# Performance work log

Measured on AMD Instinct MI355X. Metric: run time of the kernel, lower is better.

Reference implementation:

```python
import jax, jax.numpy as jnp
import numpy as np
import math

B, L, D = 8, 2048, 768
ORDER, EMB = 128, 5
FFT = 2 * L
MIN_DECAY = math.log(0.01) / 1.5   # slow_decay_pct = 1.5
MAX_DECAY = math.log(0.01) / 0.3   # fast_decay_pct = 0.3
SHIFT = 0.0


def _pos_emb(seq_len, emb_dim):
    # pos_emb_init from the source: [t, Re(z), Im(z)] with bands = (emb_dim-1)//2
    bands = (emb_dim - 1) // 2
    t = jnp.linspace(0.0, 1.0, seq_len)[None, :, None]
    t_res = jnp.linspace(0.0, seq_len - 1, seq_len)[None, :, None]
    w = 2.0 * jnp.pi * t_res / seq_len
    f = jnp.linspace(1e-4, bands - 1, bands)[None, None]
    zc = jnp.exp(-1j * f * w)
    return jnp.concatenate([t, zc.real, zc.imag], axis=-1).astype(jnp.float32)  # (1, L, EMB)


def setup_inputs() -> dict:
    key = jax.random.key(0)
    ks = jax.random.split(key, 16)
    s = 0.02
    return {
        "u": jax.random.normal(ks[0], (B, L, D), jnp.float32),
        "in_W": jax.random.normal(ks[1], (D, 3 * D), jnp.float32) * s,
        "in_b": jnp.zeros((3 * D,), jnp.float32),
        "out_W": jax.random.normal(ks[2], (D, D), jnp.float32) * s,
        "out_b": jnp.zeros((D,), jnp.float32),
        "x1_s": jax.random.normal(ks[3], (D, 4), jnp.float32) * 0.25,
        "x2_s": jax.random.normal(ks[4], (D, 4), jnp.float32) * 0.25,
        "v_s": jax.random.normal(ks[5], (D, 4), jnp.float32) * 0.25,
        "x1_sb": jax.random.normal(ks[6], (D,), jnp.float32) * 0.1,
        "x2_sb": jax.random.normal(ks[7], (D,), jnp.float32) * 0.1,
        "v_sb": jax.random.normal(ks[8], (D,), jnp.float32) * 0.1,
        "D_bias": jax.random.normal(ks[9], (D,), jnp.float32),
        "z": _pos_emb(L, EMB),
        "sin_freq": 10.0 * jnp.ones((1, ORDER), jnp.float32),   # hyena_w = 10
        "eo_mat": jax.random.normal(ks[10], (1, EMB, ORDER), jnp.float32) * 0.3,
        "eo_bias": jnp.zeros((1, ORDER), jnp.float32),
        "oo1_mat": jax.random.normal(ks[11], (1, ORDER, ORDER), jnp.float32) * 0.08,
        "oo1_bias": jnp.zeros((1, ORDER), jnp.float32),
        "oo2_mat": jax.random.normal(ks[12], (1, ORDER, ORDER), jnp.float32) * 0.08,
        "oo2_bias": jnp.zeros((1, ORDER), jnp.float32),
        "oh_mat": jax.random.normal(ks[13], (1, ORDER, D), jnp.float32) * 0.08,
    }


def _depthwise4(x, w, b):
    # torch Conv1d(groups=3D, kernel=4, padding=3) truncated to [:L] == causal conv, left pad 3
    out = jax.lax.conv_general_dilated(
        x, w[:, None, :], window_strides=(1,), padding=[(3, 0)],
        dimension_numbers=("NCH", "OIH", "NCH"), feature_group_count=x.shape[1])
    return out + b[None, :, None]


def _hyena_filter(z, sin_freq, eo_mat, eo_bias, oo1_mat, oo1_bias, oo2_mat, oo2_bias, oh_mat):
    # then exponential decay modulation (exp_mod_in_place_fwd), channels=1, reverse=0.
    f = sin_freq[:, None, :]                                       # (1, 1, ORDER)
    h = jnp.sin(f * (jnp.einsum("cle,ceo->clo", z, eo_mat) + eo_bias[:, None, :]))
    h = jnp.sin(f * (jnp.einsum("clo,cop->clp", h, oo1_mat) + oo1_bias[:, None, :]))
    h = jnp.sin(f * (jnp.einsum("clo,cop->clp", h, oo2_mat) + oo2_bias[:, None, :]))
    k = jnp.einsum("clo,coh->clh", h, oh_mat)                      # (1, L, D)
    t = jnp.linspace(0.0, 1.0, k.shape[1])
    deltas = jnp.abs(jnp.linspace(MIN_DECAY, MAX_DECAY, k.shape[2]))
    k = k * (jnp.exp(-t[None, :, None] * deltas[None, None, :]) + SHIFT)
    return k[0].T                                                  # (D, L)


def _forward(u, in_W, in_b, out_W, out_b, x1_s, x2_s, v_s, x1_sb, x2_sb, v_sb,
             D_bias, z, sin_freq, eo_mat, eo_bias, oo1_mat, oo1_bias,
             oo2_mat, oo2_bias, oh_mat):
    seqlen = u.shape[1]
    k = _hyena_filter(z, sin_freq, eo_mat, eo_bias, oo1_mat, oo1_bias, oo2_mat, oo2_bias, oh_mat)
    x1x2v = u @ in_W + in_b                                        # (B, L, 3D)
    x1, x2, v = jnp.split(x1x2v, 3, axis=-1)
    x1 = jnp.transpose(x1, (0, 2, 1))                              # (B, D, L)
    x2 = jnp.transpose(x2, (0, 2, 1))
    v = jnp.transpose(v, (0, 2, 1))
    x1 = _depthwise4(x1, x1_s, x1_sb)
    x2 = _depthwise4(x2, x2_s, x2_sb)
    v = _depthwise4(v, v_s, v_sb)
    v = v * x1                                                     # first gate
    k_f = jnp.fft.rfft(k.astype(jnp.float32), n=FFT)               # (D, FFT//2+1)
    v_f = jnp.fft.rfft(v.astype(jnp.float32), n=FFT)               # (B, D, FFT//2+1)
    y = jnp.fft.irfft(v_f * k_f[None], n=FFT)[..., :seqlen]        # long FFT conv
    y = y + v * D_bias[None, :, None]                              # skip term
    y = y * x2                                                     # second gate
    y = jnp.transpose(y, (0, 2, 1))                                # (B, L, D)
    return y @ out_W + out_b


def reference(u, in_W, in_b, out_W, out_b, x1_s, x2_s, v_s, x1_sb, x2_sb, v_sb,
              D_bias, z, sin_freq, eo_mat, eo_bias, oo1_mat, oo1_bias,
              oo2_mat, oo2_bias, oh_mat):
    return _forward(u, in_W, in_b, out_W, out_b, x1_s, x2_s, v_s, x1_sb, x2_sb, v_sb,
                    D_bias, z, sin_freq, eo_mat, eo_bias, oo1_mat, oo1_bias,
                    oo2_mat, oo2_bias, oh_mat)
```

## Files before the change

### kernel.cpp

```cpp
#include <hip/hip_runtime.h>


typedef __bf16 bf16x8 __attribute__((ext_vector_type(8)));
typedef float  f32x4  __attribute__((ext_vector_type(4)));

#define AS1 __attribute__((address_space(1)))
#define AS3 __attribute__((address_space(3)))
#define GLD16(gp, lp) __builtin_amdgcn_global_load_lds((AS1 void*)(void*)(gp), (AS3 void*)(void*)(lp), 16, 0, 0)

#define LGKM_BAR       __asm__ __volatile__("s_waitcnt lgkmcnt(0)\n\ts_barrier" ::: "memory")
#define VM_LGKM_BAR(N) __asm__ __volatile__("s_waitcnt vmcnt(" #N ") lgkmcnt(0)\n\ts_barrier" ::: "memory")

__device__ __forceinline__ unsigned short f2b(float f) {
    unsigned u = __builtin_bit_cast(unsigned, f);
    unsigned r = (u + 0x7fffu + ((u >> 16) & 1u)) >> 16;
    return (unsigned short)r;
}
__device__ __forceinline__ float b2f_lo(unsigned u) {
    return __builtin_bit_cast(float, u << 16);
}
__device__ __forceinline__ float b2f_hi(unsigned u) {
    return __builtin_bit_cast(float, u & 0xffff0000u);
}

__device__ __forceinline__ float2 cmul(float2 a, float2 b) {
    return make_float2(a.x * b.x - a.y * b.y, a.x * b.y + a.y * b.x);
}
__device__ __forceinline__ float2 cadd(float2 a, float2 b) { return make_float2(a.x + b.x, a.y + b.y); }
__device__ __forceinline__ float2 csub(float2 a, float2 b) { return make_float2(a.x - b.x, a.y - b.y); }

#define TWO_PI 6.283185307179586f

#define BFLY(i,j)   { float2 ta=x[i], tb=x[j]; x[i]=cadd(ta,tb); x[j]=csub(ta,tb); }
#define BFLYW(i,j,w){ float2 ta=x[i], tb=x[j]; x[i]=cadd(ta,tb); x[j]=cmul(csub(ta,tb),(w)); }
#define BFLYI(i,j)  { float2 ta=x[i], tb=x[j]; x[i]=cadd(ta,tb); float2 tt=csub(ta,tb); x[j]=make_float2(-dd*tt.y, dd*tt.x); }
#define CSWAP(i,j)  { float2 tt=x[i]; x[i]=x[j]; x[j]=tt; }

template<int DIR, bool UZ>
__device__ __forceinline__ void dft16(float2* x) {
    const float dd = (float)DIR;
    const float C1 = 0.92387953251128674f, S1 = 0.38268343236508977f, R2 = 0.70710678118654752f;
    const float2 W1 = make_float2( C1, dd*S1);
    const float2 W2 = make_float2( R2, dd*R2);
    const float2 W3 = make_float2( S1, dd*C1);
    const float2 W5 = make_float2(-S1, dd*C1);
    const float2 W6 = make_float2(-R2, dd*R2);
    const float2 W7 = make_float2(-C1, dd*S1);
    if (UZ) {
        x[8]  = x[0];
        x[9]  = cmul(x[1], W1);
        x[10] = cmul(x[2], W2);
        x[11] = cmul(x[3], W3);
        x[12] = make_float2(-dd*x[4].y, dd*x[4].x);
        x[13] = cmul(x[5], W5);
        x[14] = cmul(x[6], W6);
        x[15] = cmul(x[7], W7);
    } else {
        BFLY(0,8); BFLYW(1,9,W1); BFLYW(2,10,W2); BFLYW(3,11,W3);
        BFLYI(4,12); BFLYW(5,13,W5); BFLYW(6,14,W6); BFLYW(7,15,W7);
    }
    BFLY(0,4);  BFLYW(1,5,W2);  BFLYI(2,6);   BFLYW(3,7,W6);
    BFLY(8,12); BFLYW(9,13,W2); BFLYI(10,14); BFLYW(11,15,W6);
    BFLY(0,2);  BFLYI(1,3);  BFLY(4,6);   BFLYI(5,7);
    BFLY(8,10); BFLYI(9,11); BFLY(12,14); BFLYI(13,15);
    BFLY(0,1); BFLY(2,3); BFLY(4,5); BFLY(6,7);
    BFLY(8,9); BFLY(10,11); BFLY(12,13); BFLY(14,15);
    CSWAP(1,8); CSWAP(2,4); CSWAP(3,12); CSWAP(5,10); CSWAP(7,14); CSWAP(11,13);
}

__device__ __forceinline__ void twiddle16(float2* x, float ang) {
    float s, c; __sincosf(ang, &s, &c);
    const float2 u1  = make_float2(c, s);
    const float2 u2  = cmul(u1, u1);
    const float2 u3  = cmul(u2, u1);
    const float2 u4  = cmul(u2, u2);
    const float2 u8  = cmul(u4, u4);
    const float2 u12 = cmul(u8, u4);
    x[1]  = cmul(x[1],  u1);
    x[2]  = cmul(x[2],  u2);
    x[3]  = cmul(x[3],  u3);
    x[4]  = cmul(x[4],  u4);
    x[5]  = cmul(x[5],  cmul(u4, u1));
    x[6]  = cmul(x[6],  cmul(u4, u2));
    x[7]  = cmul(x[7],  cmul(u4, u3));
    x[8]  = cmul(x[8],  u8);
    x[9]  = cmul(x[9],  cmul(u8, u1));
    x[10] = cmul(x[10], cmul(u8, u2));
    x[11] = cmul(x[11], cmul(u8, u3));
    x[12] = cmul(x[12], u12);
    x[13] = cmul(x[13], cmul(u12, u1));
    x[14] = cmul(x[14], cmul(u12, u2));
    x[15] = cmul(x[15], cmul(u12, u3));
}

__device__ __forceinline__ int ph1(int row, int col) { return row * 256 + (col ^ row); }
__device__ __forceinline__ int ph2(int row, int col) { return row * 16 + (col ^ (row & 15)); }

__device__ __forceinline__ void fft4096_fwd(float2* x, float2* lds, int t) {
    dft16<-1, true>(x);
    twiddle16(x, -(float)t * (TWO_PI / 4096.0f));
    #pragma unroll
    for (int k1 = 0; k1 < 16; ++k1) lds[ph1(k1, t)] = x[k1];
    __syncthreads();
    const int hi = t >> 4, lo = t & 15;
    #pragma unroll
    for (int t1 = 0; t1 < 16; ++t1) x[t1] = lds[ph1(hi, t1 * 16 + lo)];
    dft16<-1, false>(x);
    twiddle16(x, -(float)lo * (TWO_PI / 256.0f));
    __syncthreads();
    #pragma unroll
    for (int k2 = 0; k2 < 16; ++k2) lds[ph2(t, k2)] = x[k2];
    __syncthreads();
    #pragma unroll
    for (int t0 = 0; t0 < 16; ++t0) x[t0] = lds[ph2(hi * 16 + t0, lo)];
    dft16<-1, false>(x);
}

__device__ __forceinline__ void fft4096_inv(float2* x, float2* lds, int t) {
    const int hi = t >> 4, lo = t & 15;
    dft16<1, false>(x);
    __syncthreads();
    #pragma unroll
    for (int t0 = 0; t0 < 16; ++t0) lds[ph2(hi * 16 + t0, lo)] = x[t0];
    __syncthreads();
    #pragma unroll
    for (int k2 = 0; k2 < 16; ++k2) x[k2] = lds[ph2(t, k2)];
    twiddle16(x, (float)lo * (TWO_PI / 256.0f));
    dft16<1, false>(x);
    __syncthreads();
    #pragma unroll
    for (int t1 = 0; t1 < 16; ++t1) lds[ph1(hi, t1 * 16 + lo)] = x[t1];
    __syncthreads();
    #pragma unroll
    for (int k1 = 0; k1 < 16; ++k1) x[k1] = lds[ph1(k1, t)];
    twiddle16(x, (float)t * (TWO_PI / 4096.0f));
    dft16<1, false>(x);
}

__global__ __launch_bounds__(256) void filter_k_kernel(
    const float* __restrict__ z, const float* __restrict__ sf,
    const float* __restrict__ eo, const float* __restrict__ eo_b,
    const float* __restrict__ oo1, const float* __restrict__ oo1_b,
    const float* __restrict__ oo2, const float* __restrict__ oo2_b,
    const float* __restrict__ oh, float* __restrict__ kfil)
{
    __shared__ float h3buf[4][128];
    __shared__ float htmp[2][128];
    const int t = threadIdx.x;
    const int l0 = blockIdx.x * 4;
    const int half = t >> 7;
    const int o = t & 127;
    const float sfo = sf[o];
    for (int p = 0; p < 2; ++p) {
        const int li = p * 2 + half;
        const int l = l0 + li;
        float a = eo_b[o];
        #pragma unroll
        for (int e = 0; e < 5; ++e) a += z[l * 5 + e] * eo[e * 128 + o];
        htmp[half][o] = sinf(sfo * a);
        __syncthreads();
        float a2 = oo1_b[o];
        for (int q = 0; q < 128; ++q) a2 += htmp[half][q] * oo1[q * 128 + o];
        const float h2 = sinf(sfo * a2);
        __syncthreads();
        htmp[half][o] = h2;
        __syncthreads();
        float a3 = oo2_b[o];
        for (int q = 0; q < 128; ++q) a3 += htmp[half][q] * oo2[q * 128 + o];
        h3buf[li][o] = sinf(sfo * a3);
        __syncthreads();
    }
    const float MIND = -3.070113457325394f;
    const float MAXD = -15.350567286626972f;
    for (int c = 0; c < 3; ++c) {
        const int h = t + c * 256;
        float acc[4];
        #pragma unroll
        for (int li = 0; li < 4; ++li) acc[li] = 0.f;
        for (int q = 0; q < 128; ++q) {
            const float w = oh[q * 768 + h];
            #pragma unroll
            for (int li = 0; li < 4; ++li) acc[li] += h3buf[li][q] * w;
        }
        const float delta = fabsf(MIND + (MAXD - MIND) * (float)h * (1.0f / 767.0f));
        #pragma unroll
        for (int li = 0; li < 4; ++li) {
            const int l = l0 + li;
            const float tt = (float)l * (1.0f / 2047.0f);
            kfil[h * 2048 + l] = acc[li] * expf(-tt * delta);
        }
    }
}

__global__ __launch_bounds__(256) void filter_fft_kernel(
    const float* __restrict__ kfil, const float* __restrict__ D_bias,
    float2* __restrict__ Kf)
{
    __shared__ __align__(16) float2 lds[4096];
    const int d = blockIdx.x, t = threadIdx.x;
    float2 x[16];
    #pragma unroll
    for (int r = 0; r < 8; ++r) x[r] = make_float2(kfil[d * 2048 + r * 256 + t], 0.f);
    fft4096_fwd(x, lds, t);
    const float db = D_bias[d];
    const float s = 1.0f / 4096.0f;
    #pragma unroll
    for (int k3 = 0; k3 < 16; ++k3)
        Kf[d * 4096 + k3 * 256 + t] = make_float2((x[k3].x + db) * s, x[k3].y * s);
}

__global__ __launch_bounds__(256) void convert_u_kernel(
    const float* __restrict__ u, unsigned short* __restrict__ ub)
{
    const int g = blockIdx.x * 256 + threadIdx.x;
    const float4 v = ((const float4*)u)[g];
    uint2 o;
    o.x = (unsigned)f2b(v.x) | ((unsigned)f2b(v.y) << 16);
    o.y = (unsigned)f2b(v.z) | ((unsigned)f2b(v.w) << 16);
    ((uint2*)ub)[g] = o;
}

__global__ __launch_bounds__(256) void transpose_W_kernel(
    const float* __restrict__ W, unsigned short* __restrict__ Wt, int K, int N)
{
    __shared__ float tile[32][33];
    const int n0 = blockIdx.x * 32, k0 = blockIdx.y * 32;
    const int tx = threadIdx.x & 31, ty = threadIdx.x >> 5;
    #pragma unroll
    for (int r = 0; r < 4; ++r) {
        const int kk = ty + r * 8;
        tile[kk][tx] = W[(k0 + kk) * N + n0 + tx];
    }
    __syncthreads();
    #pragma unroll
    for (int r = 0; r < 4; ++r) {
        const int nn = ty + r * 8;
        Wt[(n0 + nn) * K + k0 + tx] = f2b(tile[tx][nn]);
    }
}

__global__ __launch_bounds__(256) void transpose_Y_kernel(
    const unsigned short* __restrict__ Y, unsigned short* __restrict__ Yt)
{
    __shared__ unsigned short tile[32][34];
    const int bx = blockIdx.x;
    const int l0 = (bx & 63) * 32;
    const int tmp = bx >> 6;
    const int d0 = (tmp % 24) * 32;
    const int b  = tmp / 24;
    const int tx = threadIdx.x & 31, ty = threadIdx.x >> 5;
    #pragma unroll
    for (int r = 0; r < 4; ++r) {
        const int dd = ty + r * 8;
        tile[dd][tx] = Y[(b * 768 + d0 + dd) * 2048 + l0 + tx];
    }
    __syncthreads();
    #pragma unroll
    for (int r = 0; r < 4; ++r) {
        const int ll = ty + r * 8;
        Yt[(b * 2048 + l0 + ll) * 768 + d0 + tx] = tile[tx][ll];
    }
}

template<int TM, int TN, int WR, int WC, int MODE>
__global__ __launch_bounds__(512, 2) void gemm8ph_kernel(
    const unsigned short* __restrict__ A,
    const unsigned short* __restrict__ Bm,
    const float* __restrict__ bias,
    unsigned short* __restrict__ outb,
    float* __restrict__ outf)
{
    constexpr int MF = TM / WR / 16;
    constexpr int NF = TN / WC / 16;
    constexpr int MH = MF / 2;
    constexpr int NH = NF / 2;
    constexpr int QA = TM / 64;
    constexpr int QB = TN / 64;
    extern __shared__ __align__(16) unsigned short lds[];
    unsigned short* As = lds;
    unsigned short* Bs = lds + 2 * TM * 64;
    const int t = threadIdx.x;
    const int wv = t >> 6, lane = t & 63;
    const int row0 = (MODE == 0 ? blockIdx.y : blockIdx.x) * TM;
    const int col0 = (MODE == 0 ? blockIdx.x : blockIdx.y) * TN;
    const int wr = wv / WC, wc = wv % WC;
    const int frow = lane & 15, kc = lane >> 4;

    f32x4 acc[MF][NF] = {};

    const int srow = t >> 3;
    const int cdat = (t & 7) ^ (srow & 7);
    const unsigned short* gA = A  + (row0 + srow) * 768 + cdat * 8;
    const unsigned short* gB = Bm + (col0 + srow) * 768 + cdat * 8;

#define STG_Aq(buf, q, kt) GLD16(gA + (q) * 49152 + (kt),                     \
        (char*)As + (buf) * (TM * 128) + (q) * 8192 + wv * 1024)
#define STG_Bq(buf, q, kt) GLD16(gB + (q) * 49152 + (kt),                     \
        (char*)Bs + (buf) * (TN * 128) + (q) * 8192 + wv * 1024)
#define STG_A1(buf, kt) { STG_Aq(buf, 0, kt); STG_Aq(buf, 1, kt); }
#define STG_A2(buf, kt) { _Pragma("unroll") for (int q = 2; q < QA; ++q) STG_Aq(buf, q, kt); }
#define STG_B1(buf, kt) { STG_Bq(buf, 0, kt); STG_Bq(buf, 1, kt); }
#define STG_B2(buf, kt) { _Pragma("unroll") for (int q = 2; q < QB; ++q) STG_Bq(buf, q, kt); }
#define FENCE_QB { if constexpr (QB == 4) { VM_LGKM_BAR(4); } else { VM_LGKM_BAR(3); } }

    bf16x8 aF[MH][2], bN0[NH][2], bN1[NH][2];

#define READ_A(buf, mh)                                                        \
    _Pragma("unroll") for (int m = 0; m < MH; ++m) {                           \
        const int r = wr * (TM / WR) + ((mh) * MH + m) * 16 + frow;            \
        aF[m][0] = *(const bf16x8*)(As + (buf) * (TM * 64) + r * 64 +          \
                                    (((0 + kc) ^ (r & 7)) << 3));              \
        aF[m][1] = *(const bf16x8*)(As + (buf) * (TM * 64) + r * 64 +          \
                                    (((4 + kc) ^ (r & 7)) << 3));              \
    }
#define READ_B(buf, nh, arr)                                                   \
    _Pragma("unroll") for (int n = 0; n < NH; ++n) {                           \
        const int r = wc * (TN / WC) + ((nh) * NH + n) * 16 + frow;            \
        arr[n][0] = *(const bf16x8*)(Bs + (buf) * (TN * 64) + r * 64 +         \
                                     (((0 + kc) ^ (r & 7)) << 3));             \
        arr[n][1] = *(const bf16x8*)(Bs + (buf) * (TN * 64) + r * 64 +         \
                                     (((4 + kc) ^ (r & 7)) << 3));             \
    }
#define MFMA_Q(mh, nh, arr)                                                    \
    __builtin_amdgcn_s_setprio(1);                                             \
    _Pragma("unroll") for (int m = 0; m < MH; ++m)                             \
    _Pragma("unroll") for (int n = 0; n < NH; ++n)                             \
    _Pragma("unroll") for (int ks = 0; ks < 2; ++ks)                           \
        acc[(mh) * MH + m][(nh) * NH + n] =                                    \
            __builtin_amdgcn_mfma_f32_16x16x32_bf16(                           \
                aF[m][ks], arr[n][ks], acc[(mh) * MH + m][(nh) * NH + n],      \
                0, 0, 0);                                                      \
    __builtin_amdgcn_s_setprio(0);

    STG_A1(0, 0); STG_A2(0, 0); STG_B1(0, 0); STG_B2(0, 0);
    STG_B1(1, 64); STG_B2(1, 64);
    FENCE_QB;

    #pragma unroll 1
    for (int i = 0; i < 5; ++i) {
        const int k1 = (2 * i + 1) * 64, k2 = (2 * i + 2) * 64, k3 = (2 * i + 3) * 64;
        READ_A(0, 0); READ_B(0, 0, bN0);
        STG_A1(1, k1);
        MFMA_Q(0, 0, bN0);
        LGKM_BAR;
        READ_B(0, 1, bN1);
        STG_A2(1, k1);
        MFMA_Q(0, 1, bN1);
        LGKM_BAR;
        READ_A(0, 1);
        STG_B1(0, k2);
        MFMA_Q(1, 1, bN1);
        LGKM_BAR;
        STG_B2(0, k2);
        MFMA_Q(1, 0, bN0);
        FENCE_QB;
        READ_A(1, 0); READ_B(1, 0, bN0);
        STG_A1(0, k2);
        MFMA_Q(0, 0, bN0);
        LGKM_BAR;
        READ_B(1, 1, bN1);
        STG_A2(0, k2);
        MFMA_Q(0, 1, bN1);
        LGKM_BAR;
        READ_A(1, 1);
        STG_B1(1, k3);
        MFMA_Q(1, 1, bN1);
        LGKM_BAR;
        STG_B2(1, k3);
        MFMA_Q(1, 0, bN0);
        FENCE_QB;
    }

    {
        READ_A(0, 0); READ_B(0, 0, bN0);
        STG_A1(1, 704);
        MFMA_Q(0, 0, bN0);
        LGKM_BAR;
        READ_B(0, 1, bN1);
        STG_A2(1, 704);
        MFMA_Q(0, 1, bN1);
        LGKM_BAR;
        READ_A(0, 1);
        MFMA_Q(1, 1, bN1);
        LGKM_BAR;
        MFMA_Q(1, 0, bN0);
        VM_LGKM_BAR(0);
        READ_A(1, 0); READ_B(1, 0, bN0); READ_B(1, 1, bN1);
        MFMA_Q(0, 0, bN0);
        MFMA_Q(0, 1, bN1);
        READ_A(1, 1);
        MFMA_Q(1, 1, bN1);
        MFMA_Q(1, 0, bN0);
    }
#undef READ_A
#undef READ_B
#undef MFMA_Q
#undef STG_Aq
#undef STG_Bq
#undef STG_A1
#undef STG_A2
#undef STG_B1
#undef STG_B2
#undef FENCE_QB

    if (MODE == 0) {
        const int part = row0 / 768;
        const int bb = col0 / 2048;
        unsigned short* Xp = outb + (size_t)(part * 8 + bb) * 768 * 2048;
        const int drow0 = row0 - part * 768 + wr * (TM / WR) + kc * 4;
        const int lcol0 = col0 - bb * 2048 + wc * (TN / WC) + frow;
        #pragma unroll
        for (int m = 0; m < MF; ++m) {
            #pragma unroll
            for (int rr = 0; rr < 4; ++rr) {
                const int dd = drow0 + m * 16 + rr;
                const float bn = bias[row0 + wr * (TM / WR) + kc * 4 + m * 16 + rr];
                #pragma unroll
                for (int n = 0; n < NF; ++n)
                    Xp[dd * 2048 + lcol0 + n * 16] = f2b(acc[m][n][rr] + bn);
            }
        }
    } else {
        #pragma unroll
        for (int m = 0; m < MF; ++m) {
            #pragma unroll
            for (int rr = 0; rr < 4; ++rr) {
                const int mm = row0 + wr * (TM / WR) + kc * 4 + m * 16 + rr;
                #pragma unroll
                for (int n = 0; n < NF; ++n) {
                    const int nn = col0 + wc * (TN / WC) + n * 16 + frow;
                    outf[(size_t)mm * 768 + nn] = acc[m][n][rr] + bias[nn];
                }
            }
        }
    }
}

__device__ __forceinline__ void conv6(const unsigned short* __restrict__ p,
                                      const float* w, float bias, int t, float* out8)
{
    const uint4 m = *(const uint4*)(p + 8 * t);
    uint2 q = make_uint2(0u, 0u);
    if (t) q = *(const uint2*)(p + 8 * t - 4);
    float s[12];
    s[0] = b2f_lo(q.x); s[1] = b2f_hi(q.x); s[2] = b2f_lo(q.y); s[3] = b2f_hi(q.y);
    s[4] = b2f_lo(m.x); s[5] = b2f_hi(m.x); s[6] = b2f_lo(m.y); s[7] = b2f_hi(m.y);
    s[8] = b2f_lo(m.z); s[9] = b2f_hi(m.z); s[10] = b2f_lo(m.w); s[11] = b2f_hi(m.w);
    #pragma unroll
    for (int i = 0; i < 8; ++i)
        out8[i] = bias + w[0] * s[i + 1] + w[1] * s[i + 2] + w[2] * s[i + 3] + w[3] * s[i + 4];
}

__global__ __launch_bounds__(256) void fft_conv_kernel(
    const unsigned short* __restrict__ X, const float2* __restrict__ Kf,
    const float* __restrict__ x1_s, const float* __restrict__ x2_s, const float* __restrict__ v_s,
    const float* __restrict__ x1_sb, const float* __restrict__ x2_sb, const float* __restrict__ v_sb,
    unsigned short* __restrict__ Y)
{
    __shared__ __align__(16) float2 lds[4096];
    unsigned* ldsu = (unsigned*)lds;
    const int d = blockIdx.x, jp = blockIdx.y, t = threadIdx.x;
    const int b0 = jp * 2, b1 = b0 + 1;

    const unsigned short* px1a = X + ((size_t)(0 * 8 + b0) * 768 + d) * 2048;
    const unsigned short* pva  = X + ((size_t)(2 * 8 + b0) * 768 + d) * 2048;
    const unsigned short* px1b = X + ((size_t)(0 * 8 + b1) * 768 + d) * 2048;
    const unsigned short* pvb  = X + ((size_t)(2 * 8 + b1) * 768 + d) * 2048;

    {
        float w1[4], wv[4];
        #pragma unroll
        for (int j = 0; j < 4; ++j) { w1[j] = x1_s[d * 4 + j]; wv[j] = v_s[d * 4 + j]; }
        const float bc1 = x1_sb[d], bcv = v_sb[d];
        float pa[8];
        {
            float va[8], g[8];
            conv6(pva,  wv, bcv, t, va);
            conv6(px1a, w1, bc1, t, g);
            #pragma unroll
            for (int i = 0; i < 8; ++i) pa[i] = va[i] * g[i];
        }
        {
            float vb[8], g[8];
            conv6(pvb,  wv, bcv, t, vb);
            conv6(px1b, w1, bc1, t, g);
            unsigned vh[8];
            #pragma unroll
            for (int i = 0; i < 8; ++i)
                vh[i] = (unsigned)f2b(pa[i]) | ((unsigned)f2b(vb[i] * g[i]) << 16);
            *(uint4*)(ldsu + 8 * t)     = make_uint4(vh[0], vh[1], vh[2], vh[3]);
            *(uint4*)(ldsu + 8 * t + 4) = make_uint4(vh[4], vh[5], vh[6], vh[7]);
        }
    }
    __syncthreads();

    float2 x[16];
    #pragma unroll
    for (int r = 0; r < 8; ++r) {
        const unsigned u = ldsu[r * 256 + t];
        x[r] = make_float2(b2f_lo(u), b2f_hi(u));
    }
    __syncthreads();

    fft4096_fwd(x, lds, t);

    {
        const float2* kf = Kf + (size_t)d * 4096;
        #pragma unroll
        for (int c4 = 0; c4 < 4; ++c4) {
            float2 kr[4];
            #pragma unroll
            for (int j = 0; j < 4; ++j) kr[j] = kf[(c4 * 4 + j) * 256 + t];
            #pragma unroll
            for (int j = 0; j < 4; ++j) x[c4 * 4 + j] = cmul(x[c4 * 4 + j], kr[j]);
            __asm__ __volatile__("" ::: "memory");
        }
    }

    fft4096_inv(x, lds, t);

    __syncthreads();
    {
        const unsigned short* px2a = X + ((size_t)(1 * 8 + b0) * 768 + d) * 2048;
        const unsigned short* px2b = X + ((size_t)(1 * 8 + b1) * 768 + d) * 2048;
        float w2[4];
        #pragma unroll
        for (int j = 0; j < 4; ++j) w2[j] = x2_s[d * 4 + j];
        const float bc2 = x2_sb[d];
        float ga[8], gb[8];
        conv6(px2a, w2, bc2, t, ga);
        conv6(px2b, w2, bc2, t, gb);
        unsigned c2[8];
        #pragma unroll
        for (int i = 0; i < 8; ++i)
            c2[i] = (unsigned)f2b(ga[i]) | ((unsigned)f2b(gb[i]) << 16);
        *(uint4*)(ldsu + 8 * t)     = make_uint4(c2[0], c2[1], c2[2], c2[3]);
        *(uint4*)(ldsu + 8 * t + 4) = make_uint4(c2[4], c2[5], c2[6], c2[7]);
    }
    __syncthreads();

    unsigned short* ya = Y + ((size_t)b0 * 768 + d) * 2048;
    unsigned short* yb = Y + ((size_t)b1 * 768 + d) * 2048;
    #pragma unroll
    for (int n1 = 0; n1 < 8; ++n1) {
        const int l = n1 * 256 + t;
        const unsigned u = ldsu[l];
        ya[l] = f2b(x[n1].x * b2f_lo(u));
        yb[l] = f2b(x[n1].y * b2f_hi(u));
    }
}

extern "C" void kernel_launch(void* const* d_in, const int* in_sizes, int n_in,
                              void* d_out, int out_size, void* d_ws, size_t ws_size,
                              hipStream_t stream)
{
    (void)in_sizes; (void)n_in; (void)out_size; (void)ws_size;
    const float* u      = (const float*)d_in[0];
    const float* in_W   = (const float*)d_in[1];
    const float* in_b   = (const float*)d_in[2];
    const float* out_W  = (const float*)d_in[3];
    const float* out_b  = (const float*)d_in[4];
    const float* x1_s   = (const float*)d_in[5];
    const float* x2_s   = (const float*)d_in[6];
    const float* v_s    = (const float*)d_in[7];
    const float* x1_sb  = (const float*)d_in[8];
    const float* x2_sb  = (const float*)d_in[9];
    const float* v_sb   = (const float*)d_in[10];
    const float* D_bias = (const float*)d_in[11];
    const float* z      = (const float*)d_in[12];
    const float* sf     = (const float*)d_in[13];
    const float* eo     = (const float*)d_in[14];
    const float* eo_b   = (const float*)d_in[15];
    const float* oo1    = (const float*)d_in[16];
    const float* oo1_b  = (const float*)d_in[17];
    const float* oo2    = (const float*)d_in[18];
    const float* oo2_b  = (const float*)d_in[19];
    const float* oh     = (const float*)d_in[20];
    float* out = (float*)d_out;

    char* ws = (char*)d_ws;
    unsigned short* Xbf  = (unsigned short*)(ws + 0);
    unsigned short* Ybf  = (unsigned short*)(ws + 75497472);
    unsigned short* ubYt = (unsigned short*)(ws + 100663296);
    unsigned short* Wt   = (unsigned short*)(ws + 125829120);
    unsigned short* W2t  = (unsigned short*)(ws + 129368064);
    float*          kfil = (float*)(ws + 130547712);
    float2*         Kf   = (float2*)(ws + 136839168);

    static int attr_set = 0;
    if (!attr_set) {
        (void)hipFuncSetAttribute(
            reinterpret_cast<const void*>(&gemm8ph_kernel<192, 256, 2, 4, 0>),
            hipFuncAttributeMaxDynamicSharedMemorySize, 114688);
        (void)hipFuncSetAttribute(
            reinterpret_cast<const void*>(&gemm8ph_kernel<256, 192, 4, 2, 1>),
            hipFuncAttributeMaxDynamicSharedMemorySize, 114688);
        attr_set = 1;
    }

    filter_k_kernel<<<512, 256, 0, stream>>>(z, sf, eo, eo_b, oo1, oo1_b, oo2, oo2_b, oh, kfil);
    filter_fft_kernel<<<768, 256, 0, stream>>>(kfil, D_bias, Kf);
    convert_u_kernel<<<12288, 256, 0, stream>>>(u, ubYt);
    transpose_W_kernel<<<dim3(72, 24), 256, 0, stream>>>(in_W, Wt, 768, 2304);
    transpose_W_kernel<<<dim3(24, 24), 256, 0, stream>>>(out_W, W2t, 768, 768);
    gemm8ph_kernel<192, 256, 2, 4, 0><<<dim3(64, 12), 512, 114688, stream>>>(
        Wt, ubYt, in_b, Xbf, nullptr);
    fft_conv_kernel<<<dim3(768, 4), 256, 0, stream>>>(Xbf, Kf, x1_s, x2_s, v_s, x1_sb, x2_sb, v_sb, Ybf);
    transpose_Y_kernel<<<12288, 256, 0, stream>>>(Ybf, ubYt);
    gemm8ph_kernel<256, 192, 4, 2, 1><<<dim3(64, 4), 512, 114688, stream>>>(
        ubYt, W2t, out_b, nullptr, out);
}
```

Measured before the change: 361.3 us.

## Use a simpler two-phase double-buffered pipeline for the output projection GEMM

Splits the output-projection GEMM out of the shared 8-phase template into its own kernel. The new kernel stages full A/B tiles per k-step into two LDS buffers and interleaves the global-to-LDS loads with MFMA on the other buffer, using one barrier per half-iteration. The aim is to cut the scheduling and barrier overhead of the finer-grained 8-phase pipeline for this smaller GEMM, at the cost of coarser overlap and possibly more exposed memory latency.

After: 360.8 us. About the same (-0.1%).

```diff
diff --git a/kernel.cpp b/kernel.cpp
--- a/kernel.cpp
+++ b/kernel.cpp
@@ -262,13 +262,12 @@
     }
 }
 
-template<int TM, int TN, int WR, int WC, int MODE>
+template<int TM, int TN, int WR, int WC>
 __global__ __launch_bounds__(512, 2) void gemm8ph_kernel(
     const unsigned short* __restrict__ A,
     const unsigned short* __restrict__ Bm,
     const float* __restrict__ bias,
-    unsigned short* __restrict__ outb,
-    float* __restrict__ outf)
+    unsigned short* __restrict__ outb)
 {
     constexpr int MF = TM / WR / 16;
     constexpr int NF = TN / WC / 16;
@@ -281,8 +280,8 @@
     unsigned short* Bs = lds + 2 * TM * 64;
     const int t = threadIdx.x;
     const int wv = t >> 6, lane = t & 63;
-    const int row0 = (MODE == 0 ? blockIdx.y : blockIdx.x) * TM;
-    const int col0 = (MODE == 0 ? blockIdx.x : blockIdx.y) * TN;
+    const int row0 = blockIdx.y * TM;
+    const int col0 = blockIdx.x * TN;
     const int wr = wv / WC, wc = wv % WC;
     const int frow = lane & 15, kc = lane >> 4;
 
@@ -403,7 +402,7 @@
 #undef STG_B2
 #undef FENCE_QB
 
-    if (MODE == 0) {
+    {
         const int part = row0 / 768;
         const int bb = col0 / 2048;
         unsigned short* Xp = outb + (size_t)(part * 8 + bb) * 768 * 2048;
@@ -420,17 +419,98 @@
                     Xp[dd * 2048 + lcol0 + n * 16] = f2b(acc[m][n][rr] + bn);
             }
         }
-    } else {
-        #pragma unroll
-        for (int m = 0; m < MF; ++m) {
+    }
+}
+
+template<int TM, int TN, int WR, int WC>
+__global__ __launch_bounds__(512, 2) void gemm2ph_kernel(
+    const unsigned short* __restrict__ A,
+    const unsigned short* __restrict__ Bm,
+    const float* __restrict__ bias,
+    float* __restrict__ outf)
+{
+    constexpr int MF = TM / WR / 16;
+    constexpr int NF = TN / WC / 16;
+    constexpr int QA = TM / 64;
+    constexpr int QB = TN / 64;
+    extern __shared__ __align__(16) unsigned short lds[];
+    unsigned short* As = lds;
+    unsigned short* Bs = lds + 2 * TM * 64;
+    const int t = threadIdx.x;
+    const int wv = t >> 6, lane = t & 63;
+    const int row0 = blockIdx.x * TM;
+    const int col0 = blockIdx.y * TN;
+    const int wr = wv / WC, wc = wv % WC;
+    const int frow = lane & 15, kc = lane >> 4;
+
+    f32x4 acc[MF][NF] = {};
+
+    const int srow = t >> 3;
+    const int cdat = (t & 7) ^ (srow & 7);
+    const unsigned short* gA = A  + (row0 + srow) * 768 + cdat * 8;
+    const unsigned short* gB = Bm + (col0 + srow) * 768 + cdat * 8;
+
+#define STAGE(buf, kt)                                                        \
+    {                                                                         \
+        _Pragma("unroll") for (int q = 0; q < QA; ++q)                        \
+            GLD16(gA + q * 49152 + (kt) * 64,                                 \
+                  (char*)As + (buf) * (TM * 128) + q * 8192 + wv * 1024);     \
+        _Pragma("unroll") for (int q = 0; q < QB; ++q)                        \
+            GLD16(gB + q * 49152 + (kt) * 64,                                 \
+                  (char*)Bs + (buf) * (TN * 128) + q * 8192 + wv * 1024);     \
+    }
+
+#define HALF(buf, ks)                                                         \
+    {                                                                         \
+        bf16x8 aF[MF], bF[NF];                                                \
+        _Pragma("unroll") for (int m = 0; m < MF; ++m) {                      \
+            const int r = wr * (TM / WR) + m * 16 + frow;                     \
+            aF[m] = *(const bf16x8*)(As + (buf) * (TM * 64) + r * 64 +        \
+                                     ((((ks) * 4 + kc) ^ (r & 7)) << 3));     \
+        }                                                                     \
+        _Pragma("unroll") for (int n = 0; n < NF; ++n) {                      \
+            const int r = wc * (TN / WC) + n * 16 + frow;                     \
+            bF[n] = *(const bf16x8*)(Bs + (buf) * (TN * 64) + r * 64 +        \
+                                     ((((ks) * 4 + kc) ^ (r & 7)) << 3));     \
+        }                                                                     \
+        __builtin_amdgcn_s_setprio(1);                                        \
+        _Pragma("unroll") for (int m = 0; m < MF; ++m)                        \
+        _Pragma("unroll") for (int n = 0; n < NF; ++n)                        \
+            acc[m][n] = __builtin_amdgcn_mfma_f32_16x16x32_bf16(              \
+                aF[m], bF[n], acc[m][n], 0, 0, 0);                            \
+        __builtin_amdgcn_s_setprio(0);                                        \
+    }
+
+    STAGE(0, 0);
+    STAGE(1, 1);
+    VM_LGKM_BAR(7);
+
+    HALF(0, 0); HALF(0, 1);
+    VM_LGKM_BAR(0);
+
+    #pragma unroll 1
+    for (int kt = 1; kt <= 9; kt += 2) {
+        STAGE(0, kt + 1);
+        HALF(1, 0); HALF(1, 1);
+        VM_LGKM_BAR(0);
+        STAGE(1, kt + 2);
+        HALF(0, 0); HALF(0, 1);
+        VM_LGKM_BAR(0);
+    }
+
+    HALF(1, 0); HALF(1, 1);
+#undef STAGE
+#undef HALF
+
+    #pragma unroll
+    for (int m = 0; m < MF; ++m) {
+        #pragma unroll
+        for (int rr = 0; rr < 4; ++rr) {
+            const int mm = row0 + wr * (TM / WR) + kc * 4 + m * 16 + rr;
             #pragma unroll
-            for (int rr = 0; rr < 4; ++rr) {
-                const int mm = row0 + wr * (TM / WR) + kc * 4 + m * 16 + rr;
-                #pragma unroll
-                for (int n = 0; n < NF; ++n) {
-                    const int nn = col0 + wc * (TN / WC) + n * 16 + frow;
-                    outf[(size_t)mm * 768 + nn] = acc[m][n][rr] + bias[nn];
-                }
+            for (int n = 0; n < NF; ++n) {
+                const int nn = col0 + wc * (TN / WC) + n * 16 + frow;
+                outf[(size_t)mm * 768 + nn] = acc[m][n][rr] + bias[nn];
             }
         }
     }
@@ -590,10 +670,10 @@
     static int attr_set = 0;
     if (!attr_set) {
         (void)hipFuncSetAttribute(
-            reinterpret_cast<const void*>(&gemm8ph_kernel<192, 256, 2, 4, 0>),
+            reinterpret_cast<const void*>(&gemm8ph_kernel<192, 256, 2, 4>),
             hipFuncAttributeMaxDynamicSharedMemorySize, 114688);
         (void)hipFuncSetAttribute(
-            reinterpret_cast<const void*>(&gemm8ph_kernel<256, 192, 4, 2, 1>),
+            reinterpret_cast<const void*>(&gemm2ph_kernel<256, 192, 4, 2>),
             hipFuncAttributeMaxDynamicSharedMemorySize, 114688);
         attr_set = 1;
     }
@@ -603,10 +683,10 @@
     convert_u_kernel<<<12288, 256, 0, stream>>>(u, ubYt);
     transpose_W_kernel<<<dim3(72, 24), 256, 0, stream>>>(in_W, Wt, 768, 2304);
     transpose_W_kernel<<<dim3(24, 24), 256, 0, stream>>>(out_W, W2t, 768, 768);
-    gemm8ph_kernel<192, 256, 2, 4, 0><<<dim3(64, 12), 512, 114688, stream>>>(
-        Wt, ubYt, in_b, Xbf, nullptr);
+    gemm8ph_kernel<192, 256, 2, 4><<<dim3(64, 12), 512, 114688, stream>>>(
+        Wt, ubYt, in_b, Xbf);
     fft_conv_kernel<<<dim3(768, 4), 256, 0, stream>>>(Xbf, Kf, x1_s, x2_s, v_s, x1_sb, x2_sb, v_sb, Ybf);
     transpose_Y_kernel<<<12288, 256, 0, stream>>>(Ybf, ubYt);
-    gemm8ph_kernel<256, 192, 4, 2, 1><<<dim3(64, 4), 512, 114688, stream>>>(
-        ubYt, W2t, out_b, nullptr, out);
-}
+    gemm2ph_kernel<256, 192, 4, 2><<<dim3(64, 4), 512, 114688, stream>>>(
+        ubYt, W2t, out_b, out);
+}
```
